# Performance work log

Measured on AMD Instinct MI355X. Metric: run time of the kernel, lower is better.

Reference implementation:

```python
import jax, jax.numpy as jnp
import numpy as np


def _rotate_half(x):
    half = x.shape[-1] // 2
    x1, x2 = x[..., :half], x[..., half:]
    return jnp.concatenate([-x2, x1], axis=-1)


def setup_inputs() -> dict:
    key = jax.random.key(0)
    ks = jax.random.split(key, 7)
    B, T, D, H, Hd = 4, 2048, 1024, 16, 64
    x = jax.random.normal(ks[0], (B, T, D), dtype=jnp.float32)
    # RoPE tables (realistic: built from inv freqs)
    inv_freq = 1.0 / (10000.0 ** (jnp.arange(0, Hd, 2, dtype=jnp.float32) / Hd))
    pos = jnp.arange(T, dtype=jnp.float32)
    freqs = pos[:, None] * inv_freq[None, :]            # (T, Hd/2)
    emb = jnp.concatenate([freqs, freqs], axis=-1)       # (T, Hd)
    cos, sin = jnp.cos(emb), jnp.sin(emb)
    s = 1.0 / np.sqrt(D)
    w_q = jax.random.normal(ks[1], (D, D), dtype=jnp.float32) * s
    w_k = jax.random.normal(ks[2], (D, D), dtype=jnp.float32) * s
    w_v = jax.random.normal(ks[3], (D, D), dtype=jnp.float32) * s
    w_o = jax.random.normal(ks[4], (D, D), dtype=jnp.float32) * s
    return {"x": x, "cos": cos, "sin": sin, "w_q": w_q, "w_k": w_k, "w_v": w_v, "w_o": w_o}


def reference(x, cos, sin, w_q, w_k, w_v, w_o):
    B, T, D = x.shape
    H = 16
    Hd = D // H
    scale = Hd ** -0.5
    # nn.Linear(bias=False): y = x @ W.T
    q = (x @ w_q.T).reshape(B, T, H, Hd).transpose(0, 2, 1, 3)  # (B,H,T,Hd)
    k = (x @ w_k.T).reshape(B, T, H, Hd).transpose(0, 2, 1, 3)
    v = (x @ w_v.T).reshape(B, T, H, Hd).transpose(0, 2, 1, 3)
    c = cos[None, None, :, :]
    s = sin[None, None, :, :]
    q = q * c + _rotate_half(q) * s
    k = k * c + _rotate_half(k) * s
    scores = jnp.einsum('bhqd,bhkd->bhqk', q, k) * scale  # (B,H,T,T)
    causal = jnp.tril(jnp.ones((T, T), dtype=bool))
    scores = jnp.where(causal[None, None], scores, -jnp.inf)
    weights = jax.nn.softmax(scores, axis=-1)
    out = jnp.einsum('bhqk,bhkd->bhqd', weights, v)
    out = out.transpose(0, 2, 1, 3).reshape(B, T, D)
    return out @ w_o.T
```

## Files before the change

kernel.cpp:

```cpp
#include <hip/hip_runtime.h>
#include <stdint.h>

typedef __attribute__((ext_vector_type(8))) __bf16 bf16x8;
typedef __attribute__((ext_vector_type(4))) float floatx4;


__device__ __forceinline__ unsigned short f2bf(float f) {
    unsigned int u = __float_as_uint(f);
    u += 0x7FFFu + ((u >> 16) & 1u);
    return (unsigned short)(u >> 16);
}
__device__ __forceinline__ unsigned int pack2bf(float lo, float hi) {
    return (unsigned int)f2bf(lo) | ((unsigned int)f2bf(hi) << 16);
}
__device__ __forceinline__ unsigned int packtrunc(float lo, float hi) {
    return __builtin_amdgcn_perm(__float_as_uint(hi), __float_as_uint(lo), 0x07060302u);
}

__device__ __forceinline__ void gl_lds16(const void* g, void* l) {
    __builtin_amdgcn_global_load_lds(
        (const __attribute__((address_space(1))) void*)g,
        (__attribute__((address_space(3))) void*)l, 16, 0, 0);
}


__global__ void cvt_all(const float* __restrict__ x,  const float* __restrict__ wq,
                        const float* __restrict__ wk, const float* __restrict__ wv,
                        const float* __restrict__ wo,
                        unsigned short* __restrict__ xb,  unsigned short* __restrict__ wqb,
                        unsigned short* __restrict__ wkb, unsigned short* __restrict__ wvb,
                        unsigned short* __restrict__ wob) {
    int i = blockIdx.x * blockDim.x + threadIdx.x;
    const float* in; unsigned short* out; int idx;
    if (i < 2097152) { in = x; out = xb; idx = i; }
    else {
        int j = i - 2097152; int wsel = j >> 18; idx = j & 262143;
        in  = (wsel == 0) ? wq  : (wsel == 1) ? wk  : (wsel == 2) ? wv  : wo;
        out = (wsel == 0) ? wqb : (wsel == 1) ? wkb : (wsel == 2) ? wvb : wob;
    }
    float4 v = ((const float4*)in)[idx];
    ushort4 o;
    o.x = f2bf(v.x); o.y = f2bf(v.y); o.z = f2bf(v.z); o.w = f2bf(v.w);
    ((ushort4*)out)[idx] = o;
}


template<int MODE>
__global__ __launch_bounds__(256, 2)
void gemm_bt(const unsigned short* __restrict__ A,
             const unsigned short* __restrict__ Wq,
             const unsigned short* __restrict__ Wk,
             const float* __restrict__ cosp,
             const float* __restrict__ sinp,
             unsigned short* __restrict__ outq,
             unsigned short* __restrict__ outk,
             unsigned short* __restrict__ outvt,
             float* __restrict__ outf)
{
    constexpr int K = 1024;
    __shared__ __align__(16) unsigned short As[128 * 32];
    __shared__ __align__(16) unsigned short Bs[128 * 32];

    const int t    = threadIdx.x;
    const int w    = t >> 6;
    const int lane = t & 63;
    const int c    = lane & 15;
    const int quad = lane >> 4;
    const int wr   = w >> 1, wc = w & 1;

    const int m0 = blockIdx.x * 128;
    int which, n0;
    const unsigned short* W;
    if constexpr (MODE == 0) {
        which = blockIdx.y >> 3;
        n0    = (blockIdx.y & 7) * 128;
        W     = which ? Wk : Wq;
    } else {
        which = 0;
        n0    = blockIdx.y * 128;
        W     = Wq;
    }

    const int srow = t >> 2;
    const int scol = (t & 3) * 8;
    const unsigned short* ga0 = A + (size_t)(m0 + srow) * K + scol;
    const unsigned short* ga1 = A + (size_t)(m0 + srow + 64) * K + scol;
    const unsigned short* gb0 = W + (size_t)(n0 + srow) * K + scol;
    const unsigned short* gb1 = W + (size_t)(n0 + srow + 64) * K + scol;
    void* lA0 = (char*)As + t * 16;
    void* lA1 = (char*)As + 4096 + t * 16;
    void* lB0 = (char*)Bs + t * 16;
    void* lB1 = (char*)Bs + 4096 + t * 16;

    floatx4 acc[4][4] = {};

    const int arow = wr * 64;
    const int brow = wc * 64;

    for (int k0 = 0; k0 < K; k0 += 32) {
        __syncthreads();
        gl_lds16(ga0 + k0, lA0);
        gl_lds16(ga1 + k0, lA1);
        gl_lds16(gb0 + k0, lB0);
        gl_lds16(gb1 + k0, lB1);
        __syncthreads();
        bf16x8 af[4], bfr[4];
        #pragma unroll
        for (int mi = 0; mi < 4; mi++)
            af[mi] = *(const bf16x8*)&As[(arow + mi * 16 + c) * 32 + quad * 8];
        #pragma unroll
        for (int ni = 0; ni < 4; ni++)
            bfr[ni] = *(const bf16x8*)&Bs[(brow + ni * 16 + c) * 32 + quad * 8];
        if constexpr (MODE == 2) {
            #pragma unroll
            for (int mi = 0; mi < 4; mi++)
                #pragma unroll
                for (int ni = 0; ni < 4; ni++)
                    acc[mi][ni] = __builtin_amdgcn_mfma_f32_16x16x32_bf16(
                        af[mi], bfr[ni], acc[mi][ni], 0, 0, 0);
        } else {
            #pragma unroll
            for (int mi = 0; mi < 4; mi++)
                #pragma unroll
                for (int ni = 0; ni < 4; ni++)
                    acc[mi][ni] = __builtin_amdgcn_mfma_f32_16x16x32_bf16(
                        bfr[ni], af[mi], acc[mi][ni], 0, 0, 0);
        }
    }

    if constexpr (MODE == 1) {
        #pragma unroll
        for (int mi = 0; mi < 4; mi++) {
            int m = m0 + wr * 64 + mi * 16 + c;
            #pragma unroll
            for (int ni = 0; ni < 4; ni++) {
                int n = n0 + wc * 64 + ni * 16 + quad * 4;
                *(floatx4*)&outf[(size_t)m * 1024 + n] = acc[mi][ni];
            }
        }
    } else if constexpr (MODE == 2) {
        const int hh = (n0 + wc * 64) >> 6;
        #pragma unroll
        for (int mi = 0; mi < 4; mi++) {
            int t0 = m0 + wr * 64 + mi * 16 + quad * 4;
            int b = t0 >> 11, tt0 = t0 & 2047;
            #pragma unroll
            for (int ni = 0; ni < 4; ni++) {
                int d = ni * 16 + c;
                uint2 pk;
                pk.x = pack2bf(acc[mi][ni][0], acc[mi][ni][1]);
                pk.y = pack2bf(acc[mi][ni][2], acc[mi][ni][3]);
                *(uint2*)&outvt[((size_t)((b * 16 + hh) * 64 + d)) * 2048 + tt0] = pk;
            }
        }
    } else {
        const int hh = (n0 + wc * 64) >> 6;
        unsigned short* dst = which ? outk : outq;
        const float scale = which ? 1.0f : (0.125f * 1.44269504088896f);
        #pragma unroll
        for (int mi = 0; mi < 4; mi++) {
            int m = m0 + wr * 64 + mi * 16 + c;
            int b = m >> 11, tt = m & 2047;
            size_t obase = ((size_t)(b * 16 + hh) * 2048 + tt) * 64;
            #pragma unroll
            for (int ni = 0; ni < 4; ni++) {
                int d0 = ni * 16 + quad * 4;
                float4 cv = *(const float4*)&cosp[tt * 64 + d0];
                float4 sv = *(const float4*)&sinp[tt * 64 + d0];
                float ca[4] = {cv.x, cv.y, cv.z, cv.w};
                float sa[4] = {sv.x, sv.y, sv.z, sv.w};
                float vq[4];
                #pragma unroll
                for (int r = 0; r < 4; r++) {
                    float pr  = acc[mi][ni ^ 2][r];
                    float rot = (ni & 2) ? pr : -pr;
                    vq[r] = (acc[mi][ni][r] * ca[r] + rot * sa[r]) * scale;
                }
                uint2 pk;
                pk.x = pack2bf(vq[0], vq[1]);
                pk.y = pack2bf(vq[2], vq[3]);
                *(uint2*)&dst[obase + d0] = pk;
            }
        }
    }
}

__global__ __launch_bounds__(256)
void flash_attn(const unsigned short* __restrict__ Q,
                const unsigned short* __restrict__ Kg,
                const unsigned short* __restrict__ Vt,
                unsigned short* __restrict__ O)
{
    __shared__ __align__(16) unsigned short SMEM[40960];
    unsigned short* Ks = SMEM;
    unsigned short* Vs = SMEM + 16384;
    unsigned short* Ps = SMEM + 32768;

    const int t    = threadIdx.x;
    const int w    = t >> 6;
    const int lane = t & 63;
    const int c    = lane & 15;
    const int quad = lane >> 4;

    const int bh = blockIdx.x;
    const int b  = bh >> 4, h = bh & 15;

    const unsigned short* qp = Q  + (size_t)bh * 2048 * 64;
    const unsigned short* kp = Kg + (size_t)bh * 2048 * 64;
    const unsigned short* vp = Vt + (size_t)bh * 64 * 2048;

    const int krow = t >> 3;
    const int kblk = (t & 7) ^ (krow & 7);
    const int vrow = t >> 4;
    const int vblk = (t & 15) ^ (vrow & 15);
    unsigned short* pw = Ps + w * (64 * 32);

    const int c7  = c & 7;
    const int c3  = (c >> 1) & 3;

    for (int pp = 0; pp < 2; pp++) {
        const int qi = pp ? (31 - (int)blockIdx.y) : (int)blockIdx.y;
        const int q0 = qi * 64;

        bf16x8 qf[4][2];
        #pragma unroll
        for (int qt = 0; qt < 4; qt++)
            #pragma unroll
            for (int dc = 0; dc < 2; dc++)
                qf[qt][dc] = *(const bf16x8*)&qp[(size_t)(q0 + qt * 16 + c) * 64 + dc * 32 + quad * 8];

        floatx4 o[4][4] = {};
        float lp[4] = {};

        __syncthreads();
        #pragma unroll
        for (int ch = 0; ch < 4; ch++) {
            gl_lds16(kp + (size_t)(ch * 32 + krow) * 64 + kblk * 8,
                     (char*)Ks + ch * 4096 + t * 16);
            gl_lds16(vp + (size_t)(ch * 16 + vrow) * 2048 + vblk * 8,
                     (char*)Vs + ch * 4096 + t * 16);
        }

        const int iters = (qi >> 1) + 1;
        for (int it = 0; it < iters; it++) {
            const int cur = it & 1;
            const int kt0 = it * 128;
            __syncthreads();
            if (it + 1 < iters) {
                const int kt1 = kt0 + 128;
                #pragma unroll
                for (int ch = 0; ch < 4; ch++) {
                    gl_lds16(kp + (size_t)(kt1 + ch * 32 + krow) * 64 + kblk * 8,
                             (char*)Ks + (cur ^ 1) * 8192 * 2 + ch * 4096 + t * 16);
                    gl_lds16(vp + (size_t)(ch * 16 + vrow) * 2048 + kt1 + vblk * 8,
                             (char*)Vs + (cur ^ 1) * 8192 * 2 + ch * 4096 + t * 16);
                }
            }
            const unsigned short* KsC = Ks + cur * 8192;
            const unsigned short* VsC = Vs + cur * 8192;

            floatx4 s[2][4] = {};
            #pragma unroll
            for (int dc = 0; dc < 2; dc++) {
                const int phys = (dc * 4 + quad) ^ c7;
                bf16x8 kf[2];
                #pragma unroll
                for (int kt = 0; kt < 2; kt++)
                    kf[kt] = *(const bf16x8*)&KsC[(w * 32 + kt * 16 + c) * 64 + phys * 8];
                #pragma unroll
                for (int kt = 0; kt < 2; kt++)
                    #pragma unroll
                    for (int qt = 0; qt < 4; qt++)
                        s[kt][qt] = __builtin_amdgcn_mfma_f32_16x16x32_bf16(
                            kf[kt], qf[qt][dc], s[kt][qt], 0, 0, 0);
            }

            if (it == iters - 1) {
                #pragma unroll
                for (int kt = 0; kt < 2; kt++) {
                    int keyb = kt0 + w * 32 + kt * 16 + quad * 4;
                    #pragma unroll
                    for (int qt = 0; qt < 4; qt++) {
                        int qrow = q0 + qt * 16 + c;
                        #pragma unroll
                        for (int r = 0; r < 4; r++)
                            if (keyb + r > qrow) s[kt][qt][r] = -1e30f;
                    }
                }
            }

            #pragma unroll
            for (int kt = 0; kt < 2; kt++) {
                const int physw = (kt * 2 + (quad >> 1)) ^ c3;
                #pragma unroll
                for (int qt = 0; qt < 4; qt++) {
                    float p0 = __builtin_amdgcn_exp2f(s[kt][qt][0]);
                    float p1 = __builtin_amdgcn_exp2f(s[kt][qt][1]);
                    float p2 = __builtin_amdgcn_exp2f(s[kt][qt][2]);
                    float p3 = __builtin_amdgcn_exp2f(s[kt][qt][3]);
                    lp[qt] += (p0 + p1) + (p2 + p3);
                    uint2 pk;
                    pk.x = packtrunc(p0, p1);
                    pk.y = packtrunc(p2, p3);
                    *(uint2*)&pw[(qt * 16 + c) * 32 + physw * 8 + (quad & 1) * 4] = pk;
                }
            }

            {
                const int physp = quad ^ c3;
                const int physv = (w * 4 + quad) ^ c;
                bf16x8 vf[4], pf[4];
                #pragma unroll
                for (int dt = 0; dt < 4; dt++)
                    vf[dt] = *(const bf16x8*)&VsC[(dt * 16 + c) * 128 + physv * 8];
                #pragma unroll
                for (int qt = 0; qt < 4; qt++)
                    pf[qt] = *(const bf16x8*)&pw[(qt * 16 + c) * 32 + physp * 8];
                #pragma unroll
                for (int qt = 0; qt < 4; qt++)
                    #pragma unroll
                    for (int dt = 0; dt < 4; dt++)
                        o[qt][dt] = __builtin_amdgcn_mfma_f32_16x16x32_bf16(
                            vf[dt], pf[qt], o[qt][dt], 0, 0, 0);
            }
        }

        __syncthreads();
        float* red  = (float*)SMEM;
        float* lred = (float*)(SMEM + 32768);

        #pragma unroll
        for (int qt = 0; qt < 4; qt++) {
            int row = qt * 16 + c;
            #pragma unroll
            for (int dt = 0; dt < 4; dt++)
                *(floatx4*)&red[w * 4096 + row * 64 + ((dt * 4 + quad) ^ c) * 4] = o[qt][dt];
        }
        float ls[4];
        #pragma unroll
        for (int qt = 0; qt < 4; qt++) {
            float l = lp[qt];
            l += __shfl_xor(l, 16);
            l += __shfl_xor(l, 32);
            ls[qt] = l;
        }
        float lsel = (quad == 0) ? ls[0] : (quad == 1) ? ls[1] : (quad == 2) ? ls[2] : ls[3];
        lred[w * 64 + quad * 16 + c] = lsel;
        __syncthreads();

        const int row = w * 16 + c;
        floatx4 of[4] = {};
        #pragma unroll
        for (int j = 0; j < 4; j++)
            #pragma unroll
            for (int dt = 0; dt < 4; dt++)
                of[dt] += *(const floatx4*)&red[j * 4096 + row * 64 + ((dt * 4 + quad) ^ c) * 4];
        float l = lred[row] + lred[64 + row] + lred[128 + row] + lred[192 + row];
        float linv = __builtin_amdgcn_rcpf(l);
        size_t base = ((size_t)(b * 2048 + q0 + row)) * 1024 + h * 64;
        #pragma unroll
        for (int dt = 0; dt < 4; dt++) {
            uint2 pk;
            pk.x = pack2bf(of[dt][0] * linv, of[dt][1] * linv);
            pk.y = pack2bf(of[dt][2] * linv, of[dt][3] * linv);
            *(uint2*)&O[base + dt * 16 + quad * 4] = pk;
        }
    }
}


extern "C" void kernel_launch(void* const* d_in, const int* in_sizes, int n_in,
                              void* d_out, int out_size, void* d_ws, size_t ws_size,
                              hipStream_t stream) {
    const float* x    = (const float*)d_in[0];
    const float* cosp = (const float*)d_in[1];
    const float* sinp = (const float*)d_in[2];
    const float* wq   = (const float*)d_in[3];
    const float* wk   = (const float*)d_in[4];
    const float* wv   = (const float*)d_in[5];
    const float* wo   = (const float*)d_in[6];

    char* ws = (char*)d_ws;
    const size_t MB = 1024 * 1024;
    unsigned short* xb   = (unsigned short*)(ws + 0);
    unsigned short* attn = (unsigned short*)(ws + 0);
    unsigned short* wqb  = (unsigned short*)(ws + 16 * MB);
    unsigned short* wkb  = (unsigned short*)(ws + 18 * MB);
    unsigned short* wvb  = (unsigned short*)(ws + 20 * MB);
    unsigned short* wob  = (unsigned short*)(ws + 22 * MB);
    unsigned short* qbuf = (unsigned short*)(ws + 24 * MB);
    unsigned short* kbuf = (unsigned short*)(ws + 40 * MB);
    unsigned short* vtb  = (unsigned short*)(ws + 56 * MB);

    cvt_all<<<dim3(12288), 256, 0, stream>>>(x, wq, wk, wv, wo,
                                             xb, wqb, wkb, wvb, wob);

    gemm_bt<0><<<dim3(64, 16), 256, 0, stream>>>(xb, wqb, wkb, cosp, sinp,
                                                 qbuf, kbuf, nullptr, nullptr);
    gemm_bt<2><<<dim3(64, 8), 256, 0, stream>>>(xb, wvb, nullptr, nullptr, nullptr,
                                                nullptr, nullptr, vtb, nullptr);

    flash_attn<<<dim3(64, 16), 256, 0, stream>>>(qbuf, kbuf, vtb, attn);

    gemm_bt<1><<<dim3(64, 8), 256, 0, stream>>>(attn, wob, nullptr, nullptr, nullptr,
                                                nullptr, nullptr, nullptr, (float*)d_out);
}
```

Baseline: 291.0 us.

## Single-buffer attention K/V tiles and shrink LDS to fit more blocks per CU

The flash-attention kernel drops double buffering of K/V tiles. Each iteration now loads its tile into a single buffer and synchronizes before compute, which cuts static LDS from about 80KB to about 49KB so more workgroups can be resident per CU. The final cross-wave reduction is reworked so wave 0 keeps its own accumulators in registers and only the other three waves spill to LDS, which fits the smaller buffer. The GEMM launch bounds are raised to 3 blocks per CU. The cost is that load latency is no longer hidden by prefetch inside a block, and the GEMM may face tighter register limits.

Result: slower. 320.0 us (+9.9%).

```diff
diff --git a/kernel.cpp b/kernel.cpp
--- a/kernel.cpp
+++ b/kernel.cpp
@@ -46,7 +46,7 @@
 
 
 template<int MODE>
-__global__ __launch_bounds__(256, 2)
+__global__ __launch_bounds__(256, 3)
 void gemm_bt(const unsigned short* __restrict__ A,
              const unsigned short* __restrict__ Wq,
              const unsigned short* __restrict__ Wk,
@@ -191,10 +191,10 @@
                 const unsigned short* __restrict__ Vt,
                 unsigned short* __restrict__ O)
 {
-    __shared__ __align__(16) unsigned short SMEM[40960];
+    __shared__ __align__(16) unsigned short SMEM[25088];
     unsigned short* Ks = SMEM;
-    unsigned short* Vs = SMEM + 16384;
-    unsigned short* Ps = SMEM + 32768;
+    unsigned short* Vs = SMEM + 8192;
+    unsigned short* Ps = SMEM + 16384;
 
     const int t    = threadIdx.x;
     const int w    = t >> 6;
@@ -232,32 +232,18 @@
         floatx4 o[4][4] = {};
         float lp[4] = {};
 
-        __syncthreads();
-        #pragma unroll
-        for (int ch = 0; ch < 4; ch++) {
-            gl_lds16(kp + (size_t)(ch * 32 + krow) * 64 + kblk * 8,
-                     (char*)Ks + ch * 4096 + t * 16);
-            gl_lds16(vp + (size_t)(ch * 16 + vrow) * 2048 + vblk * 8,
-                     (char*)Vs + ch * 4096 + t * 16);
-        }
-
         const int iters = (qi >> 1) + 1;
         for (int it = 0; it < iters; it++) {
-            const int cur = it & 1;
             const int kt0 = it * 128;
             __syncthreads();
-            if (it + 1 < iters) {
-                const int kt1 = kt0 + 128;
-                #pragma unroll
-                for (int ch = 0; ch < 4; ch++) {
-                    gl_lds16(kp + (size_t)(kt1 + ch * 32 + krow) * 64 + kblk * 8,
-                             (char*)Ks + (cur ^ 1) * 8192 * 2 + ch * 4096 + t * 16);
-                    gl_lds16(vp + (size_t)(ch * 16 + vrow) * 2048 + kt1 + vblk * 8,
-                             (char*)Vs + (cur ^ 1) * 8192 * 2 + ch * 4096 + t * 16);
-                }
-            }
-            const unsigned short* KsC = Ks + cur * 8192;
-            const unsigned short* VsC = Vs + cur * 8192;
+            #pragma unroll
+            for (int ch = 0; ch < 4; ch++) {
+                gl_lds16(kp + (size_t)(kt0 + ch * 32 + krow) * 64 + kblk * 8,
+                         (char*)Ks + ch * 4096 + t * 16);
+                gl_lds16(vp + (size_t)(ch * 16 + vrow) * 2048 + kt0 + vblk * 8,
+                         (char*)Vs + ch * 4096 + t * 16);
+            }
+            __syncthreads();
 
             floatx4 s[2][4] = {};
             #pragma unroll
@@ -266,7 +252,7 @@
                 bf16x8 kf[2];
                 #pragma unroll
                 for (int kt = 0; kt < 2; kt++)
-                    kf[kt] = *(const bf16x8*)&KsC[(w * 32 + kt * 16 + c) * 64 + phys * 8];
+                    kf[kt] = *(const bf16x8*)&Ks[(w * 32 + kt * 16 + c) * 64 + phys * 8];
                 #pragma unroll
                 for (int kt = 0; kt < 2; kt++)
                     #pragma unroll
@@ -312,7 +298,7 @@
                 bf16x8 vf[4], pf[4];
                 #pragma unroll
                 for (int dt = 0; dt < 4; dt++)
-                    vf[dt] = *(const bf16x8*)&VsC[(dt * 16 + c) * 128 + physv * 8];
+                    vf[dt] = *(const bf16x8*)&Vs[(dt * 16 + c) * 128 + physv * 8];
                 #pragma unroll
                 for (int qt = 0; qt < 4; qt++)
                     pf[qt] = *(const bf16x8*)&pw[(qt * 16 + c) * 32 + physp * 8];
@@ -327,15 +313,8 @@
 
         __syncthreads();
         float* red  = (float*)SMEM;
-        float* lred = (float*)(SMEM + 32768);
-
-        #pragma unroll
-        for (int qt = 0; qt < 4; qt++) {
-            int row = qt * 16 + c;
-            #pragma unroll
-            for (int dt = 0; dt < 4; dt++)
-                *(floatx4*)&red[w * 4096 + row * 64 + ((dt * 4 + quad) ^ c) * 4] = o[qt][dt];
-        }
+        float* lred = (float*)((char*)SMEM + 49152);
+
         float ls[4];
         #pragma unroll
         for (int qt = 0; qt < 4; qt++) {
@@ -344,26 +323,39 @@
             l += __shfl_xor(l, 32);
             ls[qt] = l;
         }
-        float lsel = (quad == 0) ? ls[0] : (quad == 1) ? ls[1] : (quad == 2) ? ls[2] : ls[3];
-        lred[w * 64 + quad * 16 + c] = lsel;
+
+        if (w) {
+            #pragma unroll
+            for (int qt = 0; qt < 4; qt++) {
+                int row = qt * 16 + c;
+                #pragma unroll
+                for (int dt = 0; dt < 4; dt++)
+                    *(floatx4*)&red[(w - 1) * 4096 + row * 64 + ((dt * 4 + quad) ^ c) * 4] = o[qt][dt];
+            }
+            float lsel = (quad == 0) ? ls[0] : (quad == 1) ? ls[1] : (quad == 2) ? ls[2] : ls[3];
+            lred[(w - 1) * 64 + quad * 16 + c] = lsel;
+        }
         __syncthreads();
 
-        const int row = w * 16 + c;
-        floatx4 of[4] = {};
-        #pragma unroll
-        for (int j = 0; j < 4; j++)
-            #pragma unroll
-            for (int dt = 0; dt < 4; dt++)
-                of[dt] += *(const floatx4*)&red[j * 4096 + row * 64 + ((dt * 4 + quad) ^ c) * 4];
-        float l = lred[row] + lred[64 + row] + lred[128 + row] + lred[192 + row];
-        float linv = __builtin_amdgcn_rcpf(l);
-        size_t base = ((size_t)(b * 2048 + q0 + row)) * 1024 + h * 64;
-        #pragma unroll
-        for (int dt = 0; dt < 4; dt++) {
-            uint2 pk;
-            pk.x = pack2bf(of[dt][0] * linv, of[dt][1] * linv);
-            pk.y = pack2bf(of[dt][2] * linv, of[dt][3] * linv);
-            *(uint2*)&O[base + dt * 16 + quad * 4] = pk;
+        if (w == 0) {
+            #pragma unroll
+            for (int qt = 0; qt < 4; qt++) {
+                int row = qt * 16 + c;
+                float l = ls[qt] + lred[row] + lred[64 + row] + lred[128 + row];
+                float linv = __builtin_amdgcn_rcpf(l);
+                size_t base = ((size_t)(b * 2048 + q0 + row)) * 1024 + h * 64;
+                #pragma unroll
+                for (int dt = 0; dt < 4; dt++) {
+                    floatx4 of = o[qt][dt];
+                    #pragma unroll
+                    for (int j = 0; j < 3; j++)
+                        of += *(const floatx4*)&red[j * 4096 + row * 64 + ((dt * 4 + quad) ^ c) * 4];
+                    uint2 pk;
+                    pk.x = pack2bf(of[0] * linv, of[1] * linv);
+                    pk.y = pack2bf(of[2] * linv, of[3] * linv);
+                    *(uint2*)&O[base + dt * 16 + quad * 4] = pk;
+                }
+            }
         }
     }
 }
```
